# Optimization experiments

Measured on AMD Instinct MI355X. Metric: run time of the kernel, lower is better.

The kernel has to match this reference:

```python
import jax, jax.numpy as jnp
import numpy as np

BATCH, SEQ, D_MODEL, STATE_DIM = 16, 4096, 512, 512


def _xavier(key, shape):
    fan_in, fan_out = shape[1], shape[0]
    limit = float(np.sqrt(6.0 / (fan_in + fan_out)))
    return jax.random.uniform(key, shape, jnp.float32, -limit, limit)


def setup_inputs() -> dict:
    key = jax.random.key(0)
    kx, ka, kb, kc = jax.random.split(key, 4)
    x = jax.random.normal(kx, (BATCH, SEQ, D_MODEL), jnp.float32)
    A = _xavier(ka, (STATE_DIM, STATE_DIM))
    B = _xavier(kb, (STATE_DIM, D_MODEL))
    C = _xavier(kc, (D_MODEL, STATE_DIM))
    return {"x": x, "A": A, "B": B, "C": C}


def reference(x, A, B, C):
    # x: [batch, seq, d_model]; state: [batch, state_dim]
    batch = x.shape[0]
    state0 = jnp.zeros((batch, A.shape[0]), x.dtype)

    # Precompute input projection for all timesteps: [seq, batch, state_dim]
    bx = jnp.einsum('btd,nd->tbn', x, B)

    def step(state, bx_t):
        # state_{t} = relu(state_{t-1} @ A^T + B @ x_t)
        state = jax.nn.relu(state @ A.T + bx_t)
        y = state @ C.T  # [batch, d_model]
        return state, y

    _, ys = jax.lax.scan(step, state0, bx)
    return jnp.transpose(ys, (1, 0, 2))  # [batch, seq, d_model]
```

## Files before the change

kernel.cpp:

```cpp
#include <hip/hip_runtime.h>
#include <hip/hip_bf16.h>

typedef __attribute__((ext_vector_type(4))) float  fvec4;
typedef __attribute__((ext_vector_type(8))) short  svec8;
typedef __attribute__((ext_vector_type(8))) unsigned short usvec8;
typedef __attribute__((ext_vector_type(4))) unsigned short usvec4;
typedef __attribute__((ext_vector_type(4))) unsigned int   uivec4;

#define MFMA16 __builtin_amdgcn_mfma_f32_16x16x32_bf16

static __device__ __forceinline__ unsigned short f2bf(float f) {
    __hip_bfloat16 h = __float2bfloat16(f);
    return __builtin_bit_cast(unsigned short, h);
}
static __device__ __forceinline__ float bf2f(unsigned short u) {
    unsigned int v = ((unsigned int)u) << 16;
    return __builtin_bit_cast(float, v);
}

__global__ void cvt_kernel(const float* __restrict__ in, unsigned short* __restrict__ out, int n4) {
    int stride = gridDim.x * blockDim.x;
    for (int i = blockIdx.x * blockDim.x + threadIdx.x; i < n4; i += stride) {
        fvec4 v = ((const fvec4*)in)[i];
        usvec4 u;
        u[0] = f2bf(v[0]); u[1] = f2bf(v[1]); u[2] = f2bf(v[2]); u[3] = f2bf(v[3]);
        ((usvec4*)out)[i] = u;
    }
}

template<bool LHS_F32_PERM, bool OUT_PERM>
__global__ __launch_bounds__(256)
void gemm512(const void* __restrict__ lhsv, const unsigned short* __restrict__ rhs,
             void* __restrict__ outv)
{
    __shared__ __align__(16) unsigned short smA[64 * 72];
    __shared__ __align__(16) unsigned short smB[64 * 72];
    const int tid = threadIdx.x;
    const int m0 = blockIdx.x * 64;
    const int n0 = blockIdx.y * 64;
    const int w = tid >> 6, l = tid & 63;
    const int g = l >> 4, r16 = l & 15;
    const int wm = (w >> 1) * 32, wn = (w & 1) * 32;
    const int ri = tid >> 2;
    const int kseg = (tid & 3) * 16;

    fvec4 acc[2][2] = {};

    for (int k0 = 0; k0 < 512; k0 += 64) {
        if (LHS_F32_PERM) {
            const float* x = (const float*)lhsv;
            int m = m0 + ri;
            size_t base = ((size_t)(m & 15) * 4096 + (size_t)(m >> 4)) * 512 + k0 + kseg;
            usvec8 o0, o1;
            fvec4 v0 = *(const fvec4*)(x + base + 0);
            fvec4 v1 = *(const fvec4*)(x + base + 4);
            fvec4 v2 = *(const fvec4*)(x + base + 8);
            fvec4 v3 = *(const fvec4*)(x + base + 12);
            o0[0]=f2bf(v0[0]); o0[1]=f2bf(v0[1]); o0[2]=f2bf(v0[2]); o0[3]=f2bf(v0[3]);
            o0[4]=f2bf(v1[0]); o0[5]=f2bf(v1[1]); o0[6]=f2bf(v1[2]); o0[7]=f2bf(v1[3]);
            o1[0]=f2bf(v2[0]); o1[1]=f2bf(v2[1]); o1[2]=f2bf(v2[2]); o1[3]=f2bf(v2[3]);
            o1[4]=f2bf(v3[0]); o1[5]=f2bf(v3[1]); o1[6]=f2bf(v3[2]); o1[7]=f2bf(v3[3]);
            *(usvec8*)(smA + ri * 72 + kseg)     = o0;
            *(usvec8*)(smA + ri * 72 + kseg + 8) = o1;
        } else {
            const unsigned short* s = (const unsigned short*)lhsv;
            size_t base = (size_t)(m0 + ri) * 512 + k0 + kseg;
            *(usvec8*)(smA + ri * 72 + kseg)     = *(const usvec8*)(s + base);
            *(usvec8*)(smA + ri * 72 + kseg + 8) = *(const usvec8*)(s + base + 8);
        }
        {
            size_t base = (size_t)(n0 + ri) * 512 + k0 + kseg;
            *(usvec8*)(smB + ri * 72 + kseg)     = *(const usvec8*)(rhs + base);
            *(usvec8*)(smB + ri * 72 + kseg + 8) = *(const usvec8*)(rhs + base + 8);
        }
        __syncthreads();
        #pragma unroll
        for (int kt = 0; kt < 2; ++kt) {
            svec8 a0 = *(const svec8*)(smA + (wm +      r16) * 72 + 32 * kt + 8 * g);
            svec8 a1 = *(const svec8*)(smA + (wm + 16 + r16) * 72 + 32 * kt + 8 * g);
            svec8 b0 = *(const svec8*)(smB + (wn +      r16) * 72 + 32 * kt + 8 * g);
            svec8 b1 = *(const svec8*)(smB + (wn + 16 + r16) * 72 + 32 * kt + 8 * g);
            acc[0][0] = MFMA16(a0, b0, acc[0][0], 0, 0, 0);
            acc[0][1] = MFMA16(a0, b1, acc[0][1], 0, 0, 0);
            acc[1][0] = MFMA16(a1, b0, acc[1][0], 0, 0, 0);
            acc[1][1] = MFMA16(a1, b1, acc[1][1], 0, 0, 0);
        }
        __syncthreads();
    }
    #pragma unroll
    for (int mt = 0; mt < 2; ++mt)
    #pragma unroll
    for (int nt = 0; nt < 2; ++nt)
    #pragma unroll
    for (int r = 0; r < 4; ++r) {
        int m = m0 + wm + 16 * mt + 4 * g + r;
        int n = n0 + wn + 16 * nt + r16;
        float v = acc[mt][nt][r];
        if (OUT_PERM) {
            float* out = (float*)outv;
            out[((size_t)(m & 15) * 4096 + (size_t)(m >> 4)) * 512 + n] = v;
        } else {
            unsigned short* out = (unsigned short*)outv;
            out[(size_t)m * 512 + n] = f2bf(v);
        }
    }
}

#define RT 4096

#define LDSB(KT) (*(const svec8*)(stp + ((64 * (KT) + 16 * g) ^ swz)))
#define LDSA(J, KT) (*(const svec8*)(ldsA + (((w * 2 + (J)) * 16 + (KT)) << 9) + l * 8))

#define MFA(ACC, AF, SB) asm("v_mfma_f32_16x16x32_bf16 %0, %1, %2, %0" : "+v"(ACC) : "a"(AF), "v"(SB))
#define MFV(ACC, AF, SB) asm("v_mfma_f32_16x16x32_bf16 %0, %1, %2, %0" : "+v"(ACC) : "v"(AF), "v"(SB))

#define KTSTEP(KT) do { \
    sbv[((KT) + 2) % 3] = LDSB((KT) + 2); \
    s6a[((KT) + 2) % 3] = LDSA(0, (KT) + 2); \
    s7a[((KT) + 2) % 3] = LDSA(1, (KT) + 2); \
    svec8 sc = sbv[(KT) % 3]; \
    MFA(acc[0], af_a[KT][0], sc); \
    MFA(acc[1], af_a[KT][1], sc); \
    MFA(acc[2], af_a[KT][2], sc); \
    MFA(acc[3], af_a[KT][3], sc); \
    MFV(acc[4], af_v[KT][0], sc); \
    MFV(acc[5], af_v[KT][1], sc); \
    MFV(acc[6], s6a[(KT) % 3], sc); \
    MFV(acc[7], s7a[(KT) % 3], sc); \
    __builtin_amdgcn_sched_barrier(0); \
} while (0)

#define KTSTEPNP(KT) do { \
    svec8 sc = sbv[(KT) % 3]; \
    MFA(acc[0], af_a[KT][0], sc); \
    MFA(acc[1], af_a[KT][1], sc); \
    MFA(acc[2], af_a[KT][2], sc); \
    MFA(acc[3], af_a[KT][3], sc); \
    MFV(acc[4], af_v[KT][0], sc); \
    MFV(acc[5], af_v[KT][1], sc); \
    MFV(acc[6], s6a[(KT) % 3], sc); \
    MFV(acc[7], s7a[(KT) % 3], sc); \
    __builtin_amdgcn_sched_barrier(0); \
} while (0)

__global__ __launch_bounds__(256, 1)
void recur1cu_kernel(const unsigned short* __restrict__ Abf,
                     const unsigned short* __restrict__ bx,
                     unsigned short* __restrict__ states)
{
    __shared__ __align__(16) unsigned short st[16 * 512];
    __shared__ __align__(16) unsigned short ldsA[4 * 2 * 16 * 512];
    const int tid = threadIdx.x;
    const int w = tid >> 6, l = tid & 63;
    const int g = l >> 4, r16 = l & 15;
    const int nbase = w * 128;
    const int swz = (r16 & 7) << 4;

    #pragma unroll
    for (int j = 0; j < 2; ++j)
        #pragma unroll
        for (int kt = 0; kt < 16; ++kt) {
            usvec8 v = *(const usvec8*)(Abf + (size_t)(nbase + 16 * (6 + j) + r16) * 512
                                        + 32 * kt + 8 * g);
            *(usvec8*)(ldsA + (((w * 2 + j) * 16 + kt) << 9) + l * 8) = v;
        }

    svec8 af_a[16][4];
    #pragma unroll
    for (int kt = 0; kt < 16; ++kt)
        #pragma unroll
        for (int mt = 0; mt < 4; ++mt)
            af_a[kt][mt] = *(const svec8*)(Abf + (size_t)(nbase + 16 * mt + r16) * 512
                                           + 32 * kt + 8 * g);

    svec8 af_v[16][2];
    #pragma unroll
    for (int kt = 0; kt < 16; ++kt)
        #pragma unroll
        for (int j = 0; j < 2; ++j)
            af_v[kt][j] = *(const svec8*)(Abf + (size_t)(nbase + 16 * (4 + j) + r16) * 512
                                          + 32 * kt + 8 * g);

    __syncthreads();

    {
        const unsigned short* bp = bx + (size_t)r16 * 512 + nbase + 4 * g;
        char* stq = (char*)st + r16 * 1024;
        #pragma unroll
        for (int mt = 0; mt < 8; ++mt) {
            unsigned long long u = *(const unsigned long long*)(bp + 16 * mt);
            usvec4 o;
            #pragma unroll
            for (int r = 0; r < 4; ++r)
                o[r] = f2bf(fmaxf(bf2f((unsigned short)((u >> (16 * r)) & 0xffffu)), 0.0f));
            *(usvec4*)(stq + ((2 * (nbase + 16 * mt + 4 * g)) ^ swz)) = o;
        }
    }
    __syncthreads();

    const int erow = 4 * w + (l >> 4);
    const int eswz = (erow & 7) << 4;
    const int ecol = (l & 15) * 16;

    #pragma unroll 1
    for (int t = 1; t < RT; ++t) {
        {
            const char* sp = (const char*)st + erow * 1024;
            char* gp = (char*)states + ((size_t)(t - 1) * 16 + erow) * 1024 + ecol;
            #pragma unroll
            for (int jj = 0; jj < 4; ++jj) {
                uivec4 v = *(const uivec4*)(sp + ((ecol + 256 * jj) ^ eswz));
                *(uivec4*)(gp + 256 * jj) = v;
            }
        }

        unsigned long long bq[8];
        {
            const unsigned short* bp = bx + ((size_t)t * 16 + r16) * 512 + nbase + 4 * g;
            #pragma unroll
            for (int mt = 0; mt < 8; ++mt)
                bq[mt] = *(const unsigned long long*)(bp + 16 * mt);
        }

        fvec4 acc[8];
        #pragma unroll
        for (int mt = 0; mt < 8; ++mt) acc[mt] = fvec4{0.f, 0.f, 0.f, 0.f};
        asm volatile("s_nop 1"
                     : "+v"(acc[0]), "+v"(acc[1]), "+v"(acc[2]), "+v"(acc[3]),
                       "+v"(acc[4]), "+v"(acc[5]), "+v"(acc[6]), "+v"(acc[7]));

        const char* stp = (const char*)st + r16 * 1024;
        svec8 sbv[3], s6a[3], s7a[3];
        sbv[0] = LDSB(0); sbv[1] = LDSB(1);
        s6a[0] = LDSA(0, 0); s6a[1] = LDSA(0, 1);
        s7a[0] = LDSA(1, 0); s7a[1] = LDSA(1, 1);
        KTSTEP(0);  KTSTEP(1);  KTSTEP(2);  KTSTEP(3);
        KTSTEP(4);  KTSTEP(5);  KTSTEP(6);  KTSTEP(7);
        KTSTEP(8);  KTSTEP(9);  KTSTEP(10); KTSTEP(11);
        KTSTEP(12); KTSTEP(13); KTSTEPNP(14); KTSTEPNP(15);

        asm volatile("s_nop 7\n\ts_nop 7"
                     : "+v"(acc[0]), "+v"(acc[1]), "+v"(acc[2]), "+v"(acc[3]),
                       "+v"(acc[4]), "+v"(acc[5]), "+v"(acc[6]), "+v"(acc[7]));

        __syncthreads();

        {
            char* stq = (char*)st + r16 * 1024;
            #pragma unroll
            for (int mt = 0; mt < 8; ++mt) {
                unsigned long long u = bq[mt];
                usvec4 o;
                #pragma unroll
                for (int r = 0; r < 4; ++r) {
                    float b = bf2f((unsigned short)((u >> (16 * r)) & 0xffffu));
                    o[r] = f2bf(fmaxf(acc[mt][r] + b, 0.0f));
                }
                *(usvec4*)(stq + ((2 * (nbase + 16 * mt + 4 * g)) ^ swz)) = o;
            }
        }
        __syncthreads();
    }

    {
        const char* sp = (const char*)st + erow * 1024;
        char* gp = (char*)states + ((size_t)(RT - 1) * 16 + erow) * 1024 + ecol;
        #pragma unroll
        for (int jj = 0; jj < 4; ++jj) {
            uivec4 v = *(const uivec4*)(sp + ((ecol + 256 * jj) ^ eswz));
            *(uivec4*)(gp + 256 * jj) = v;
        }
    }
}

extern "C" void kernel_launch(void* const* d_in, const int* in_sizes, int n_in,
                              void* d_out, int out_size, void* d_ws, size_t ws_size,
                              hipStream_t stream) {
    const float* x = (const float*)d_in[0];
    const float* A = (const float*)d_in[1];
    const float* B = (const float*)d_in[2];
    const float* C = (const float*)d_in[3];
    float* out = (float*)d_out;

    char* ws = (char*)d_ws;
    unsigned short* Abf = (unsigned short*)(ws + 0);
    unsigned short* Bbf = (unsigned short*)(ws + (size_t)(1 << 19));
    unsigned short* Cbf = (unsigned short*)(ws + (size_t)(2 << 19));
    unsigned short* bx  = (unsigned short*)(ws + (size_t)(4 << 19));
    unsigned short* states = (unsigned short*)(ws + (size_t)(4 << 19) + ((size_t)1 << 26));

    cvt_kernel<<<64, 256, 0, stream>>>(A, Abf, 512 * 512 / 4);
    cvt_kernel<<<64, 256, 0, stream>>>(B, Bbf, 512 * 512 / 4);
    cvt_kernel<<<64, 256, 0, stream>>>(C, Cbf, 512 * 512 / 4);

    dim3 grid(1024, 8);
    gemm512<true, false><<<grid, 256, 0, stream>>>((const void*)x, Bbf, (void*)bx);
    recur1cu_kernel<<<1, 256, 0, stream>>>(Abf, bx, states);
    gemm512<false, true><<<grid, 256, 0, stream>>>((const void*)states, Cbf, (void*)out);
}
```

Measured before the change: 7.275 ms.

## Double-buffer recurrent state in LDS and drop one barrier per timestep

The state buffer in shared memory is double-buffered by timestep parity, so the new state can be written without first waiting on a barrier, leaving one __syncthreads per step instead of two. Global state writes now come straight from registers after the epilogue rather than via an LDS readback at the start of the next step. The bf16 packing uses v_cvt_pk_bf16_f32 inline asm. This trades extra LDS space and narrower 8-byte global stores for fewer barriers and LDS reads on the serial critical path.

```diff
diff --git a/kernel.cpp b/kernel.cpp
--- a/kernel.cpp
+++ b/kernel.cpp
@@ -5,6 +5,7 @@
 typedef __attribute__((ext_vector_type(8))) short  svec8;
 typedef __attribute__((ext_vector_type(8))) unsigned short usvec8;
 typedef __attribute__((ext_vector_type(4))) unsigned short usvec4;
+typedef __attribute__((ext_vector_type(2))) unsigned int   uivec2;
 typedef __attribute__((ext_vector_type(4))) unsigned int   uivec4;
 
 #define MFMA16 __builtin_amdgcn_mfma_f32_16x16x32_bf16
@@ -148,7 +149,7 @@
                      const unsigned short* __restrict__ bx,
                      unsigned short* __restrict__ states)
 {
-    __shared__ __align__(16) unsigned short st[16 * 512];
+    __shared__ __align__(16) unsigned short st[2][16 * 512];
     __shared__ __align__(16) unsigned short ldsA[4 * 2 * 16 * 512];
     const int tid = threadIdx.x;
     const int w = tid >> 6, l = tid & 63;
@@ -181,39 +182,30 @@
             af_v[kt][j] = *(const svec8*)(Abf + (size_t)(nbase + 16 * (4 + j) + r16) * 512
                                           + 32 * kt + 8 * g);
 
-    __syncthreads();
-
     {
         const unsigned short* bp = bx + (size_t)r16 * 512 + nbase + 4 * g;
-        char* stq = (char*)st + r16 * 1024;
+        char* stq = (char*)&st[0][0] + r16 * 1024;
+        unsigned short* gout = states + (size_t)r16 * 512;
         #pragma unroll
         for (int mt = 0; mt < 8; ++mt) {
             unsigned long long u = *(const unsigned long long*)(bp + 16 * mt);
-            usvec4 o;
-            #pragma unroll
-            for (int r = 0; r < 4; ++r)
-                o[r] = f2bf(fmaxf(bf2f((unsigned short)((u >> (16 * r)) & 0xffffu)), 0.0f));
-            *(usvec4*)(stq + ((2 * (nbase + 16 * mt + 4 * g)) ^ swz)) = o;
+            float f0 = fmaxf(bf2f((unsigned short)( u        & 0xffffu)), 0.0f);
+            float f1 = fmaxf(bf2f((unsigned short)((u >> 16) & 0xffffu)), 0.0f);
+            float f2 = fmaxf(bf2f((unsigned short)((u >> 32) & 0xffffu)), 0.0f);
+            float f3 = fmaxf(bf2f((unsigned short)((u >> 48) & 0xffffu)), 0.0f);
+            unsigned int plo, phi;
+            asm("v_cvt_pk_bf16_f32 %0, %1, %2" : "=v"(plo) : "v"(f0), "v"(f1));
+            asm("v_cvt_pk_bf16_f32 %0, %1, %2" : "=v"(phi) : "v"(f2), "v"(f3));
+            uivec2 ov; ov[0] = plo; ov[1] = phi;
+            int ncol = nbase + 16 * mt + 4 * g;
+            *(uivec2*)(stq + ((2 * ncol) ^ swz)) = ov;
+            *(uivec2*)(gout + ncol) = ov;
         }
     }
     __syncthreads();
-
-    const int erow = 4 * w + (l >> 4);
-    const int eswz = (erow & 7) << 4;
-    const int ecol = (l & 15) * 16;
 
     #pragma unroll 1
     for (int t = 1; t < RT; ++t) {
-        {
-            const char* sp = (const char*)st + erow * 1024;
-            char* gp = (char*)states + ((size_t)(t - 1) * 16 + erow) * 1024 + ecol;
-            #pragma unroll
-            for (int jj = 0; jj < 4; ++jj) {
-                uivec4 v = *(const uivec4*)(sp + ((ecol + 256 * jj) ^ eswz));
-                *(uivec4*)(gp + 256 * jj) = v;
-            }
-        }
-
         unsigned long long bq[8];
         {
             const unsigned short* bp = bx + ((size_t)t * 16 + r16) * 512 + nbase + 4 * g;
@@ -229,7 +221,7 @@
                      : "+v"(acc[0]), "+v"(acc[1]), "+v"(acc[2]), "+v"(acc[3]),
                        "+v"(acc[4]), "+v"(acc[5]), "+v"(acc[6]), "+v"(acc[7]));
 
-        const char* stp = (const char*)st + r16 * 1024;
+        const char* stp = (const char*)&st[(t - 1) & 1][0] + r16 * 1024;
         svec8 sbv[3], s6a[3], s7a[3];
         sbv[0] = LDSB(0); sbv[1] = LDSB(1);
         s6a[0] = LDSA(0, 0); s6a[1] = LDSA(0, 1);
@@ -243,32 +235,32 @@
                      : "+v"(acc[0]), "+v"(acc[1]), "+v"(acc[2]), "+v"(acc[3]),
                        "+v"(acc[4]), "+v"(acc[5]), "+v"(acc[6]), "+v"(acc[7]));
 
-        __syncthreads();
-
-        {
-            char* stq = (char*)st + r16 * 1024;
+        uivec2 o[8];
+        {
+            char* stq = (char*)&st[t & 1][0] + r16 * 1024;
             #pragma unroll
             for (int mt = 0; mt < 8; ++mt) {
                 unsigned long long u = bq[mt];
-                usvec4 o;
-                #pragma unroll
-                for (int r = 0; r < 4; ++r) {
-                    float b = bf2f((unsigned short)((u >> (16 * r)) & 0xffffu));
-                    o[r] = f2bf(fmaxf(acc[mt][r] + b, 0.0f));
-                }
-                *(usvec4*)(stq + ((2 * (nbase + 16 * mt + 4 * g)) ^ swz)) = o;
+                float f0 = fmaxf(acc[mt][0] + bf2f((unsigned short)( u        & 0xffffu)), 0.0f);
+                float f1 = fmaxf(acc[mt][1] + bf2f((unsigned short)((u >> 16) & 0xffffu)), 0.0f);
+                float f2 = fmaxf(acc[mt][2] + bf2f((unsigned short)((u >> 32) & 0xffffu)), 0.0f);
+                float f3 = fmaxf(acc[mt][3] + bf2f((unsigned short)((u >> 48) & 0xffffu)), 0.0f);
+                unsigned int plo, phi;
+                asm("v_cvt_pk_bf16_f32 %0, %1, %2" : "=v"(plo) : "v"(f0), "v"(f1));
+                asm("v_cvt_pk_bf16_f32 %0, %1, %2" : "=v"(phi) : "v"(f2), "v"(f3));
+                uivec2 ov; ov[0] = plo; ov[1] = phi;
+                o[mt] = ov;
+                *(uivec2*)(stq + ((2 * (nbase + 16 * mt + 4 * g)) ^ swz)) = ov;
             }
         }
+
         __syncthreads();
-    }
-
-    {
-        const char* sp = (const char*)st + erow * 1024;
-        char* gp = (char*)states + ((size_t)(RT - 1) * 16 + erow) * 1024 + ecol;
-        #pragma unroll
-        for (int jj = 0; jj < 4; ++jj) {
-            uivec4 v = *(const uivec4*)(sp + ((ecol + 256 * jj) ^ eswz));
-            *(uivec4*)(gp + 256 * jj) = v;
+
+        {
+            unsigned short* gout = states + ((size_t)t * 16 + r16) * 512;
+            #pragma unroll
+            for (int mt = 0; mt < 8; ++mt)
+                *(uivec2*)(gout + nbase + 16 * mt + 4 * g) = o[mt];
         }
     }
 }
```

New measurement: 9.866 ms. 35.6% more time.
